# Kernel tuning notes

Hardware: AMD Instinct MI355X
Metric: run time of the kernel (lower is better)

The kernel has to match this reference:

```python
import jax, jax.numpy as jnp
import numpy as np

REPARAM_OFFSET = 2.0 ** -18
PEDESTAL = REPARAM_OFFSET ** 2            # 2**-36
BETA_MIN = 1e-6
BOUND_BETA = float(np.sqrt(BETA_MIN + PEDESTAL))
BOUND_A = float(np.sqrt(0.0 + PEDESTAL))


def nn_reparam(p, bound):
    # NonNegativeParametrizer.forward: lower_bound(p, bound)**2 - pedestal
    return jnp.maximum(p, bound) ** 2 - PEDESTAL


def setup_inputs() -> dict:
    key = jax.random.key(0)
    kx, ka = jax.random.split(key)
    C, R = 192, 8
    x = jax.random.normal(kx, (8, C, 256, 256), dtype=jnp.float32)
    # parameters stored in reparam-init space: init(v) = sqrt(max(v + ped, ped))
    beta = jnp.sqrt(jnp.ones((C,), jnp.float32) + PEDESTAL)
    A = jnp.sqrt(0.1 * jax.random.uniform(ka, (C, R), dtype=jnp.float32) + PEDESTAL)
    return {"x": x, "beta": beta, "A": A}


def reference(x, beta, A):
    beta_r = nn_reparam(beta, BOUND_BETA)[None, :, None, None]   # [1,C,1,1]
    A_r = nn_reparam(A, BOUND_A)                                  # [C,r]
    x2 = x * x
    T = jnp.einsum('nchw,cr->nrhw', x2, A_r)                      # low-rank projection
    denom_sq = jnp.einsum('cr,nrhw->nchw', A_r, T) + beta_r
    return x * jax.lax.rsqrt(denom_sq)                            # inverse=False -> rsqrt
```

## Files before the change

kernel.cpp:

```cpp
#include <hip/hip_runtime.h>


#define N_IMG 8
#define C_CH 192
#define R_RK 8
#define HW 65536
#define PXB 128
#define CSLICES 8
#define CPT (C_CH / CSLICES)
#define NTHR 512
#define BLOCKS_PER_IMG (HW / PXB)

#define PEDESTAL_F 1.4551915228366852e-11f
#define BOUND_A_F 3.814697265625e-06f
#define BOUND_BETA_F 1.0000072759311364e-03f

typedef float v2 __attribute__((ext_vector_type(2)));

__global__ __launch_bounds__(NTHR, 6) void lrgdn_kernel(
    const float* __restrict__ x,
    const float* __restrict__ beta,
    const float* __restrict__ A,
    float* __restrict__ out)
{
    __shared__ float sA[C_CH][R_RK];
    __shared__ float sB[C_CH];
    __shared__ v2 sT[CSLICES][R_RK][64];

    const int tid = threadIdx.x;

    for (int i = tid; i < C_CH * R_RK; i += NTHR) {
        float a = fmaxf(A[i], BOUND_A_F);
        sA[i >> 3][i & 7] = a * a - PEDESTAL_F;
    }
    for (int i = tid; i < C_CH; i += NTHR) {
        float b = fmaxf(beta[i], BOUND_BETA_F);
        sB[i] = b * b - PEDESTAL_F;
    }
    __syncthreads();

    const int blk  = blockIdx.x;
    const int n    = blk / BLOCKS_PER_IMG;
    const int p0   = (blk % BLOCKS_PER_IMG) * PXB;
    const int lane = tid & 63;
    const int cs   = tid >> 6;
    const int c0   = cs * CPT;

    const float* xn = x   + (size_t)n * (C_CH * HW) + p0 + (size_t)c0 * HW + 2 * lane;
    float*       on = out + (size_t)n * (C_CH * HW) + p0 + (size_t)c0 * HW + 2 * lane;

    v2 xr[CPT];
#pragma unroll
    for (int i = 0; i < CPT; ++i) {
        xr[i] = *reinterpret_cast<const v2*>(xn + (size_t)i * HW);
    }

    v2 T[R_RK];
#pragma unroll
    for (int r = 0; r < R_RK; ++r) T[r] = (v2)0.f;

#pragma unroll
    for (int i = 0; i < CPT; ++i) {
        v2 s = xr[i] * xr[i];
#pragma unroll
        for (int r = 0; r < R_RK; ++r) {
            T[r] += s * sA[c0 + i][r];
        }
    }

#pragma unroll
    for (int r = 0; r < R_RK; ++r) {
        sT[cs][r][lane] = T[r];
    }
    __syncthreads();

    if (cs < 4) {
#pragma unroll
        for (int r = 0; r < R_RK; ++r) {
            T[r] += sT[cs + 4][r][lane];
            sT[cs][r][lane] = T[r];
        }
    }
    __syncthreads();

#pragma unroll
    for (int r = 0; r < R_RK; ++r) {
        v2 a01 = sT[0][r][lane] + sT[1][r][lane];
        v2 a23 = sT[2][r][lane] + sT[3][r][lane];
        T[r] = a01 + a23;
    }

#pragma unroll
    for (int i = 0; i < CPT; ++i) {
        int c = c0 + i;
        v2 d;
        d.x = sB[c];
        d.y = d.x;
#pragma unroll
        for (int r = 0; r < R_RK; ++r) {
            d += sA[c][r] * T[r];
        }
        v2 o;
        o.x = xr[i].x * __builtin_amdgcn_rsqf(d.x);
        o.y = xr[i].y * __builtin_amdgcn_rsqf(d.y);
        __builtin_nontemporal_store(o, reinterpret_cast<v2*>(on + (size_t)i * HW));
    }
}

extern "C" void kernel_launch(void* const* d_in, const int* in_sizes, int n_in,
                              void* d_out, int out_size, void* d_ws, size_t ws_size,
                              hipStream_t stream) {
    const float* x    = (const float*)d_in[0];
    const float* beta = (const float*)d_in[1];
    const float* A    = (const float*)d_in[2];
    float* out = (float*)d_out;

    dim3 grid(N_IMG * BLOCKS_PER_IMG);
    dim3 block(NTHR);
    hipLaunchKernelGGL(lrgdn_kernel, grid, block, 0, stream, x, beta, A, out);
}
```

Measured before the change: 188.2 us.

## Drop register caching of x, re-read from memory, raise occupancy to 8 waves

The kernel no longer holds all 24 channel values of x per thread in registers. It reads x from global memory twice, once for the projection and once for the output, and raises the launch-bounds occupancy hint from 6 to 8. The two-stage shared-memory reduction of T becomes a single reduction over all 8 slices, which removes one barrier. The aim is more waves in flight to hide memory latency, at the cost of a second read of x that may hit in cache or may double HBM traffic.

Measured after the change: 206.2 us. 1.1x slower.

```diff
diff --git a/kernel.cpp b/kernel.cpp
--- a/kernel.cpp
+++ b/kernel.cpp
@@ -17,7 +17,7 @@
 
 typedef float v2 __attribute__((ext_vector_type(2)));
 
-__global__ __launch_bounds__(NTHR, 6) void lrgdn_kernel(
+__global__ __launch_bounds__(NTHR, 8) void lrgdn_kernel(
     const float* __restrict__ x,
     const float* __restrict__ beta,
     const float* __restrict__ A,
@@ -33,9 +33,9 @@
         float a = fmaxf(A[i], BOUND_A_F);
         sA[i >> 3][i & 7] = a * a - PEDESTAL_F;
     }
-    for (int i = tid; i < C_CH; i += NTHR) {
-        float b = fmaxf(beta[i], BOUND_BETA_F);
-        sB[i] = b * b - PEDESTAL_F;
+    if (tid < C_CH) {
+        float b = fmaxf(beta[tid], BOUND_BETA_F);
+        sB[tid] = b * b - PEDESTAL_F;
     }
     __syncthreads();
 
@@ -49,19 +49,14 @@
     const float* xn = x   + (size_t)n * (C_CH * HW) + p0 + (size_t)c0 * HW + 2 * lane;
     float*       on = out + (size_t)n * (C_CH * HW) + p0 + (size_t)c0 * HW + 2 * lane;
 
-    v2 xr[CPT];
-#pragma unroll
-    for (int i = 0; i < CPT; ++i) {
-        xr[i] = *reinterpret_cast<const v2*>(xn + (size_t)i * HW);
-    }
-
     v2 T[R_RK];
 #pragma unroll
     for (int r = 0; r < R_RK; ++r) T[r] = (v2)0.f;
 
-#pragma unroll
+#pragma unroll 8
     for (int i = 0; i < CPT; ++i) {
-        v2 s = xr[i] * xr[i];
+        v2 v = *reinterpret_cast<const v2*>(xn + (size_t)i * HW);
+        v2 s = v * v;
 #pragma unroll
         for (int r = 0; r < R_RK; ++r) {
             T[r] += s * sA[c0 + i][r];
@@ -74,25 +69,19 @@
     }
     __syncthreads();
 
-    if (cs < 4) {
-#pragma unroll
-        for (int r = 0; r < R_RK; ++r) {
-            T[r] += sT[cs + 4][r][lane];
-            sT[cs][r][lane] = T[r];
-        }
-    }
-    __syncthreads();
-
 #pragma unroll
     for (int r = 0; r < R_RK; ++r) {
         v2 a01 = sT[0][r][lane] + sT[1][r][lane];
         v2 a23 = sT[2][r][lane] + sT[3][r][lane];
-        T[r] = a01 + a23;
+        v2 a45 = sT[4][r][lane] + sT[5][r][lane];
+        v2 a67 = sT[6][r][lane] + sT[7][r][lane];
+        T[r] = (a01 + a23) + (a45 + a67);
     }
 
-#pragma unroll
+#pragma unroll 8
     for (int i = 0; i < CPT; ++i) {
         int c = c0 + i;
+        v2 v = *reinterpret_cast<const v2*>(xn + (size_t)i * HW);
         v2 d;
         d.x = sB[c];
         d.y = d.x;
@@ -101,8 +90,8 @@
             d += sA[c][r] * T[r];
         }
         v2 o;
-        o.x = xr[i].x * __builtin_amdgcn_rsqf(d.x);
-        o.y = xr[i].y * __builtin_amdgcn_rsqf(d.y);
+        o.x = v.x * __builtin_amdgcn_rsqf(d.x);
+        o.y = v.y * __builtin_amdgcn_rsqf(d.y);
         __builtin_nontemporal_store(o, reinterpret_cast<v2*>(on + (size_t)i * HW));
     }
 }
```
